# Optimization experiments

Measured on AMD Instinct MI355X. Metric: run time of the kernel, lower is better.

Reference implementation:

```python
import jax, jax.numpy as jnp
import numpy as np

S = 8192   # seq_len (== max_seq_len)
K = 4096   # in_features
N = 4096   # out_features


def setup_inputs() -> dict:
    key = jax.random.key(0)
    k1, k2, k3, k4, k5 = jax.random.split(key, 5)
    # symmetric int8 activations and weights in [-127, 127]
    x = jax.random.randint(k1, (S, K), -127, 128, dtype=jnp.int32).astype(jnp.int8)
    weight_q = jax.random.randint(k2, (N, K), -127, 128, dtype=jnp.int32).astype(jnp.int8)
    # positive dequant scales (per-row symmetric quant: scale = absmax/127)
    scale_x = jax.random.uniform(k3, (S,), minval=0.5, maxval=2.0, dtype=jnp.float32) / 127.0
    scale_w = jax.random.uniform(k4, (N,), minval=0.5, maxval=2.0, dtype=jnp.float32) / 127.0
    # per-output-row requantization scale from the MinMax observer
    scale_y = jax.random.uniform(k5, (S,), minval=0.5, maxval=2.0, dtype=jnp.float32)
    return {"x": x, "weight_q": weight_q, "scale_x": scale_x,
            "scale_w": scale_w, "scale_y": scale_y}


def reference(x, weight_q, scale_x, scale_w, scale_y):
    # int8 GEMM with int32 accumulation: acc[s, n] = sum_k x[s, k] * w[n, k]
    acc = jnp.matmul(x.astype(jnp.int32), weight_q.T.astype(jnp.int32))  # [S, N] int32
    # fused three-scale dequant + requant: (acc * sx[s] * sw[n]) / sy[s]
    scale = (scale_x / scale_y)[:, None] * scale_w[None, :]               # [S, N]
    out_f = acc.astype(jnp.float32) * scale
    out_q = jnp.clip(jnp.round(out_f), -128.0, 127.0).astype(jnp.int8)    # int8 output
    return out_q, scale_y
```

## Files before the change

kernel.cpp:

```cpp
#include <hip/hip_runtime.h>
#include <stdint.h>

#define S_DIM 8192
#define K_DIM 4096
#define N_DIM 4096

#define BM 128
#define BN 256
#define BKB 64
#define NT (K_DIM / BKB)
#define RD 3

typedef int v4i __attribute__((ext_vector_type(4)));

__global__ void prep(const int* __restrict__ x, const int* __restrict__ w,
                     const float* __restrict__ sy,
                     int* __restrict__ dst, float* __restrict__ out) {
    const int nx = S_DIM * K_DIM / 4;
    const int nw = N_DIM * K_DIM / 4;
    int i = blockIdx.x * 256 + threadIdx.x;
    if (i < nx) {
        int4 a = ((const int4*)x)[i];
        dst[i] = (a.x & 0xFF) | ((a.y & 0xFF) << 8) | ((a.z & 0xFF) << 16)
               | ((a.w & 0xFF) << 24);
    } else if (i < nx + nw) {
        int4 a = ((const int4*)w)[i - nx];
        dst[i] = (a.x & 0xFF) | ((a.y & 0xFF) << 8) | ((a.z & 0xFF) << 16)
               | ((a.w & 0xFF) << 24);
    } else {
        int j = i - nx - nw;
        if (j < S_DIM) out[(size_t)S_DIM * N_DIM + j] = sy[j];
    }
}

__global__ void copy_sy(const float* __restrict__ sy, float* __restrict__ out) {
    int i = blockIdx.x * blockDim.x + threadIdx.x;
    if (i < S_DIM) out[(size_t)S_DIM * N_DIM + i] = sy[i];
}

__device__ __forceinline__ void g2lds16(const void* g, void* l) {
    __builtin_amdgcn_global_load_lds((const __attribute__((address_space(1))) void*)g,
                                     (__attribute__((address_space(3))) void*)l,
                                     16, 0, 0);
}

__launch_bounds__(256, 2)
__global__ void gemm_i8(const signed char* __restrict__ xp,
                        const signed char* __restrict__ wp,
                        const float* __restrict__ sx,
                        const float* __restrict__ sw,
                        const float* __restrict__ sy,
                        float* __restrict__ out) {
    __shared__ __align__(16) signed char As[RD][BM * BKB];
    __shared__ __align__(16) signed char Bs[RD][BN * BKB];

    const int tid  = threadIdx.x;
    const int lane = tid & 63;
    const int quad = lane >> 4;
    const int l16  = lane & 15;
    const int wave = tid >> 6;
    const int wm = wave >> 1;
    const int wn = wave & 1;
    const int bn = blockIdx.x;
    const int bm = blockIdx.y;

    const signed char* aG = xp + (size_t)(bm * BM) * K_DIM;
    const signed char* bG = wp + (size_t)(bn * BN) * K_DIM;

    int aOff[2], bOff[4];
#pragma unroll
    for (int i = 0; i < 2; i++) {
        int L = i * 256 + tid;
        int s = L >> 3, p = (L & 7) ^ (s & 7);
        aOff[i] = (2 * s + (p >> 2)) * K_DIM + ((p & 3) << 4);
    }
#pragma unroll
    for (int i = 0; i < 4; i++) {
        int L = i * 256 + tid;
        int s = L >> 3, p = (L & 7) ^ (s & 7);
        bOff[i] = (2 * s + (p >> 2)) * K_DIM + ((p & 3) << 4);
    }

    const int rdo = ((l16 >> 1) * 128)
                  + (((((l16 & 1) << 2) | quad) ^ (l16 >> 1)) << 4);

#define STAGE(T, SL) do { const int kk_ = (T) * BKB;                        \
        signed char* da_ = &As[SL][0];                                      \
        signed char* db_ = &Bs[SL][0];                                      \
        g2lds16(aG + aOff[0] + kk_, da_ + tid * 16);                        \
        g2lds16(aG + aOff[1] + kk_, da_ + 4096 + tid * 16);                 \
        g2lds16(bG + bOff[0] + kk_, db_ + tid * 16);                        \
        g2lds16(bG + bOff[1] + kk_, db_ + 4096 + tid * 16);                 \
        g2lds16(bG + bOff[2] + kk_, db_ + 8192 + tid * 16);                 \
        g2lds16(bG + bOff[3] + kk_, db_ + 12288 + tid * 16);                \
    } while (0)

    v4i acc[4][8];
#pragma unroll
    for (int i = 0; i < 4; i++)
#pragma unroll
        for (int j = 0; j < 8; j++) acc[i][j] = 0;

    STAGE(0, 0);
    STAGE(1, 1);

    int cs = 0;
    for (int t = 0; t < NT; ++t) {
        __builtin_amdgcn_s_barrier();
        __builtin_amdgcn_sched_barrier(0);
        int ns = cs + 2; if (ns >= RD) ns -= RD;
        if (t + 2 < NT) STAGE(t + 2, ns);
        __builtin_amdgcn_sched_barrier(0);
        if (t < NT - 2)       asm volatile("s_waitcnt vmcnt(12)" ::: "memory");
        else if (t == NT - 2) asm volatile("s_waitcnt vmcnt(6)" ::: "memory");
        else                  asm volatile("s_waitcnt vmcnt(0)" ::: "memory");
        __builtin_amdgcn_s_barrier();
        __builtin_amdgcn_sched_barrier(0);

        const signed char* a_lds = &As[cs][0] + wm * 4096 + rdo;
        const signed char* b_lds = &Bs[cs][0] + wn * 8192 + rdo;
        v4i af[4], bf[8];
#pragma unroll
        for (int mt = 0; mt < 4; mt++)
            af[mt] = *(const v4i*)(a_lds + mt * 1024);
#pragma unroll
        for (int nt = 0; nt < 8; nt++)
            bf[nt] = *(const v4i*)(b_lds + nt * 1024);
#pragma unroll
        for (int mt = 0; mt < 4; mt++)
#pragma unroll
            for (int nt = 0; nt < 8; nt++)
                acc[mt][nt] = __builtin_amdgcn_mfma_i32_16x16x64_i8(
                    af[mt], bf[nt], acc[mt][nt], 0, 0, 0);

        cs++; if (cs >= RD) cs = 0;
    }
#undef STAGE

    const int s_base = bm * BM + wm * 64;
    const int n_base = bn * BN + wn * 128;
#pragma unroll
    for (int mt = 0; mt < 4; mt++) {
#pragma unroll
        for (int r = 0; r < 4; r++) {
            int s = s_base + mt * 16 + quad * 4 + r;
            float rs = sx[s] / sy[s];
            float* orow = out + (size_t)s * N_DIM;
#pragma unroll
            for (int nt = 0; nt < 8; nt++) {
                int n = n_base + nt * 16 + l16;
                float v = rintf((float)acc[mt][nt][r] * (rs * sw[n]));
                v = fminf(fmaxf(v, -128.f), 127.f);
                orow[n] = v;
            }
        }
    }
}

__global__ void gemm_naive(const int* __restrict__ x, const int* __restrict__ w,
                           const float* __restrict__ sx, const float* __restrict__ sw,
                           const float* __restrict__ sy, float* __restrict__ out) {
    int n = blockIdx.x * blockDim.x + threadIdx.x;
    int s = blockIdx.y;
    const int4* xr = (const int4*)(x + (size_t)s * K_DIM);
    const int4* wr = (const int4*)(w + (size_t)n * K_DIM);
    int acc = 0;
    for (int k = 0; k < K_DIM / 4; k++) {
        int4 a = xr[k], b = wr[k];
        acc += a.x * b.x + a.y * b.y + a.z * b.z + a.w * b.w;
    }
    float v = rintf((float)acc * (sx[s] / sy[s] * sw[n]));
    out[(size_t)s * N_DIM + n] = fminf(fmaxf(v, -128.f), 127.f);
}

extern "C" void kernel_launch(void* const* d_in, const int* in_sizes, int n_in,
                              void* d_out, int out_size, void* d_ws, size_t ws_size,
                              hipStream_t stream) {
    const int*   x  = (const int*)d_in[0];
    const int*   wq = (const int*)d_in[1];
    const float* sx = (const float*)d_in[2];
    const float* sw = (const float*)d_in[3];
    const float* sy = (const float*)d_in[4];
    float* out = (float*)d_out;

    const size_t need = (size_t)S_DIM * K_DIM + (size_t)N_DIM * K_DIM;
    if (ws_size >= need) {
        signed char* xp = (signed char*)d_ws;
        signed char* wp = xp + (size_t)S_DIM * K_DIM;
        const int nprep = (S_DIM * K_DIM / 4) + (N_DIM * K_DIM / 4) + S_DIM;
        prep<<<dim3((nprep + 255) / 256), dim3(256), 0, stream>>>(
            x, wq, sy, (int*)xp, out);
        gemm_i8<<<dim3(N_DIM / BN, S_DIM / BM), dim3(256), 0, stream>>>(
            xp, wp, sx, sw, sy, out);
    } else {
        copy_sy<<<dim3((S_DIM + 255) / 256), dim3(256), 0, stream>>>(sy, out);
        gemm_naive<<<dim3(N_DIM / 256, S_DIM), dim3(256), 0, stream>>>(
            x, wq, sx, sw, sy, out);
    }
}
```

Measured before the change: 407.7 us.

## Replace triple-buffered async LDS pipeline with single-buffer loop and higher occupancy

Drops the 3-stage LDS ring with manual vmcnt waits and prefetch two tiles ahead. Each K-step now loads one tile into a single LDS buffer between two __syncthreads calls. Launch bounds rise from 2 to 4 blocks per CU. The aim is to rely on more resident blocks to hide global latency instead of software prefetch. In exchange, loads within a block no longer overlap with MFMA work, and the tighter register budget may cause spills given the 128-int accumulator tile.

Measured after the change: 1.575 ms. 286% more time.

```diff
diff --git a/kernel.cpp b/kernel.cpp
--- a/kernel.cpp
+++ b/kernel.cpp
@@ -9,7 +9,6 @@
 #define BN 256
 #define BKB 64
 #define NT (K_DIM / BKB)
-#define RD 3
 
 typedef int v4i __attribute__((ext_vector_type(4)));
 
@@ -44,15 +43,15 @@
                                      16, 0, 0);
 }
 
-__launch_bounds__(256, 2)
+__launch_bounds__(256, 4)
 __global__ void gemm_i8(const signed char* __restrict__ xp,
                         const signed char* __restrict__ wp,
                         const float* __restrict__ sx,
                         const float* __restrict__ sw,
                         const float* __restrict__ sy,
                         float* __restrict__ out) {
-    __shared__ __align__(16) signed char As[RD][BM * BKB];
-    __shared__ __align__(16) signed char Bs[RD][BN * BKB];
+    __shared__ __align__(16) signed char As[BM * BKB];
+    __shared__ __align__(16) signed char Bs[BN * BKB];
 
     const int tid  = threadIdx.x;
     const int lane = tid & 63;
@@ -84,41 +83,26 @@
     const int rdo = ((l16 >> 1) * 128)
                   + (((((l16 & 1) << 2) | quad) ^ (l16 >> 1)) << 4);
 
-#define STAGE(T, SL) do { const int kk_ = (T) * BKB;                        \
-        signed char* da_ = &As[SL][0];                                      \
-        signed char* db_ = &Bs[SL][0];                                      \
-        g2lds16(aG + aOff[0] + kk_, da_ + tid * 16);                        \
-        g2lds16(aG + aOff[1] + kk_, da_ + 4096 + tid * 16);                 \
-        g2lds16(bG + bOff[0] + kk_, db_ + tid * 16);                        \
-        g2lds16(bG + bOff[1] + kk_, db_ + 4096 + tid * 16);                 \
-        g2lds16(bG + bOff[2] + kk_, db_ + 8192 + tid * 16);                 \
-        g2lds16(bG + bOff[3] + kk_, db_ + 12288 + tid * 16);                \
-    } while (0)
-
     v4i acc[4][8];
 #pragma unroll
     for (int i = 0; i < 4; i++)
 #pragma unroll
         for (int j = 0; j < 8; j++) acc[i][j] = 0;
 
-    STAGE(0, 0);
-    STAGE(1, 1);
+    const signed char* a_lds = As + wm * 4096 + rdo;
+    const signed char* b_lds = Bs + wn * 8192 + rdo;
 
-    int cs = 0;
     for (int t = 0; t < NT; ++t) {
-        __builtin_amdgcn_s_barrier();
-        __builtin_amdgcn_sched_barrier(0);
-        int ns = cs + 2; if (ns >= RD) ns -= RD;
-        if (t + 2 < NT) STAGE(t + 2, ns);
-        __builtin_amdgcn_sched_barrier(0);
-        if (t < NT - 2)       asm volatile("s_waitcnt vmcnt(12)" ::: "memory");
-        else if (t == NT - 2) asm volatile("s_waitcnt vmcnt(6)" ::: "memory");
-        else                  asm volatile("s_waitcnt vmcnt(0)" ::: "memory");
-        __builtin_amdgcn_s_barrier();
-        __builtin_amdgcn_sched_barrier(0);
+        const int kk = t * BKB;
+        __syncthreads();
+        g2lds16(aG + aOff[0] + kk, As + tid * 16);
+        g2lds16(aG + aOff[1] + kk, As + 4096 + tid * 16);
+        g2lds16(bG + bOff[0] + kk, Bs + tid * 16);
+        g2lds16(bG + bOff[1] + kk, Bs + 4096 + tid * 16);
+        g2lds16(bG + bOff[2] + kk, Bs + 8192 + tid * 16);
+        g2lds16(bG + bOff[3] + kk, Bs + 12288 + tid * 16);
+        __syncthreads();
 
-        const signed char* a_lds = &As[cs][0] + wm * 4096 + rdo;
-        const signed char* b_lds = &Bs[cs][0] + wn * 8192 + rdo;
         v4i af[4], bf[8];
 #pragma unroll
         for (int mt = 0; mt < 4; mt++)
@@ -132,10 +116,7 @@
             for (int nt = 0; nt < 8; nt++)
                 acc[mt][nt] = __builtin_amdgcn_mfma_i32_16x16x64_i8(
                     af[mt], bf[nt], acc[mt][nt], 0, 0, 0);
-
-        cs++; if (cs >= RD) cs = 0;
     }
-#undef STAGE
 
     const int s_base = bm * BM + wm * 64;
     const int n_base = bn * BN + wn * 128;
```
